# Performance work log

Hardware: AMD Instinct MI355X
Metric: run time of the kernel (lower is better)

Reference implementation:

```python
import jax, jax.numpy as jnp
import numpy as np

U = 100000   # num_users
I = 50000    # num_items
N = U + I    # total nodes
D = 64       # embed_size
L = 3        # n_layers
E = 2000000  # num edges
EPS = 1e-12  # F.normalize default eps


def setup_inputs() -> dict:
    key = jax.random.key(0)
    k1, k2, k3, k4 = jax.random.split(key, 4)
    user_emb = jax.random.normal(k1, (U, D), dtype=jnp.float32) * 0.1
    item_emb = jax.random.normal(k2, (I, D), dtype=jnp.float32) * 0.1
    rows = jax.random.randint(k3, (E,), 0, N, dtype=jnp.int32)
    cols = jax.random.randint(k4, (E,), 0, N, dtype=jnp.int32)
    return {"user_emb": user_emb, "item_emb": item_emb, "rows": rows, "cols": cols}


def _spmm(vals, rows, cols, x):
    # sparse [N,N] @ dense [N,D] via gather + segment reduce
    return jax.ops.segment_sum(vals[:, None] * x[cols], rows, num_segments=N)


def _l2norm(x):
    return x / jnp.maximum(jnp.linalg.norm(x, axis=1, keepdims=True), EPS)


def reference(user_emb, item_emb, rows, cols):
    emb0 = jnp.concatenate([user_emb, item_emb], axis=0)  # [N, D]

    # laplacian_adj: G = D^-1/2 A D^-1/2 on the same edge set
    deg = jax.ops.segment_sum(jnp.ones((E,), emb0.dtype), rows, num_segments=N)
    d_is = jnp.where(deg > 0, deg ** -0.5, 0.0)
    g_vals = d_is[rows] * d_is[cols]  # [E]

    cur = emb0
    acc = emb0
    user_fine, item_fine = [], []
    for _ in range(L):
        gnn = _spmm(g_vals, rows, cols, cur)  # [N, D]
        # fine_laplacian_adj: cosine-sim edge scores, row-normalized
        gr = _l2norm(gnn[rows])
        gc = _l2norm(gnn[cols])
        scores = (jnp.sum(gr * gc, axis=1) + 1.0) * 0.5  # [E] in [0,1]
        rowsum = jax.ops.segment_sum(scores, rows, num_segments=N)
        d_inv = jnp.where(rowsum > 0, 1.0 / rowsum, 0.0)
        fine = _spmm(d_inv[rows] * scores, rows, cols, cur)  # [N, D]
        cur = gnn + fine
        acc = acc + cur
        user_fine.append(fine[:U])
        item_fine.append(fine[U:])

    u_embs = acc[:U]
    i_embs = acc[U:]
    return (u_embs, i_embs, jnp.stack(user_fine, 0), jnp.stack(item_fine, 0))
```

## Files before the change

kernel.cpp:

```cpp
#include <hip/hip_runtime.h>

namespace {

typedef unsigned short u16;
typedef __attribute__((__ext_vector_type__(2))) float f32x2;

constexpr int Un = 100000;
constexpr int In = 50000;
constexpr int Nn = 150000;
constexpr int D  = 64;
constexpr int Ln = 3;
constexpr int En = 2000000;
constexpr int CHUNK = 1024;
constexpr int NB = (Nn + CHUNK - 1) / CHUNK;

__device__ __forceinline__ u16 f2bf(float f) {
    unsigned u = __float_as_uint(f);
    unsigned r = (u + 0x7FFFu + ((u >> 16) & 1u)) >> 16;
    return (u16)r;
}
__device__ __forceinline__ float bflo(unsigned u) {
    return __uint_as_float(u << 16);
}
__device__ __forceinline__ float bfhi(unsigned u) {
    return __uint_as_float(u & 0xFFFF0000u);
}
__device__ __forceinline__ unsigned pack2(float lo, float hi) {
    return (unsigned)f2bf(lo) | ((unsigned)f2bf(hi) << 16);
}

__device__ __forceinline__ f32x2 pkfma(f32x2 a, f32x2 b, f32x2 c) {
    f32x2 d;
    asm("v_pk_fma_f32 %0, %1, %2, %3" : "=v"(d) : "v"(a), "v"(b), "v"(c));
    return d;
}

__device__ __forceinline__ float dpp_add8(float x) {
    x += __uint_as_float((unsigned)__builtin_amdgcn_update_dpp(
        0, (int)__float_as_uint(x), 0xB1, 0xF, 0xF, true));
    x += __uint_as_float((unsigned)__builtin_amdgcn_update_dpp(
        0, (int)__float_as_uint(x), 0x4E, 0xF, 0xF, true));
    x += __uint_as_float((unsigned)__builtin_amdgcn_update_dpp(
        0, (int)__float_as_uint(x), 0x141, 0xF, 0xF, true));
    return x;
}

__device__ __forceinline__ void unp8(uint4 q, f32x2* o) {
    o[0].x = bflo(q.x); o[0].y = bfhi(q.x);
    o[1].x = bflo(q.y); o[1].y = bfhi(q.y);
    o[2].x = bflo(q.z); o[2].y = bfhi(q.z);
    o[3].x = bflo(q.w); o[3].y = bfhi(q.w);
}

__global__ void count_kernel(const int* __restrict__ rows, int* __restrict__ deg,
                             int* __restrict__ eoff) {
    int e = blockIdx.x * blockDim.x + threadIdx.x;
    if (e < En) eoff[e] = atomicAdd(&deg[rows[e]], 1);
}

__global__ void scan_partial(const int* __restrict__ deg, float* __restrict__ d_is,
                             int* __restrict__ bsum) {
    int tid = threadIdx.x;
    int base = blockIdx.x * CHUNK + tid * 4;
    int s = 0;
#pragma unroll
    for (int i = 0; i < 4; ++i) {
        int idx = base + i;
        if (idx < Nn) {
            int d = deg[idx];
            s += d;
            d_is[idx] = d > 0 ? rsqrtf((float)d) : 0.f;
        }
    }
    __shared__ int sh[256];
    sh[tid] = s;
    __syncthreads();
    for (int o = 128; o > 0; o >>= 1) {
        if (tid < o) sh[tid] += sh[tid + o];
        __syncthreads();
    }
    if (tid == 0) bsum[blockIdx.x] = sh[0];
}

__global__ void scan_top(int* __restrict__ bsum, int* __restrict__ row_ptr) {
    __shared__ int sh[256];
    int tid = threadIdx.x;
    int v = (tid < NB) ? bsum[tid] : 0;
    sh[tid] = v;
    __syncthreads();
    for (int o = 1; o < 256; o <<= 1) {
        int t = (tid >= o) ? sh[tid - o] : 0;
        __syncthreads();
        sh[tid] += t;
        __syncthreads();
    }
    if (tid < NB) bsum[tid] = sh[tid] - v;
    if (tid == 255) row_ptr[Nn] = sh[255];
}

__global__ void scan_final(const int* __restrict__ deg, const int* __restrict__ bsum,
                           int* __restrict__ row_ptr) {
    int tid = threadIdx.x;
    int base = blockIdx.x * CHUNK + tid * 4;
    int v[4];
    int ts = 0;
#pragma unroll
    for (int i = 0; i < 4; ++i) {
        int idx = base + i;
        v[i] = (idx < Nn) ? deg[idx] : 0;
        ts += v[i];
    }
    __shared__ int sh[256];
    sh[tid] = ts;
    __syncthreads();
    for (int o = 1; o < 256; o <<= 1) {
        int t = (tid >= o) ? sh[tid - o] : 0;
        __syncthreads();
        sh[tid] += t;
        __syncthreads();
    }
    int excl = bsum[blockIdx.x] + sh[tid] - ts;
#pragma unroll
    for (int i = 0; i < 4; ++i) {
        int idx = base + i;
        if (idx < Nn) row_ptr[idx] = excl;
        excl += v[i];
    }
}

__global__ void fill_kernel(const int* __restrict__ rows, const int* __restrict__ cols,
                            const int* __restrict__ row_ptr, const int* __restrict__ eoff,
                            int* __restrict__ col_off) {
    int e = blockIdx.x * blockDim.x + threadIdx.x;
    if (e >= En) return;
    col_off[row_ptr[rows[e]] + eoff[e]] = cols[e] << 7;
}

__global__ void init_kernel(const float* __restrict__ ue, const float* __restrict__ ie,
                            float* __restrict__ out, u16* __restrict__ cur) {
    int i = (blockIdx.x * 256 + threadIdx.x) * 4;
    if (i >= Nn * D) return;
    const float* src = (i < Un * D) ? (ue + i) : (ie + (i - Un * D));
    float4 v = *(const float4*)src;
    *(float4*)(out + i) = v;
    ushort4 q;
    q.x = f2bf(v.x); q.y = f2bf(v.y); q.z = f2bf(v.z); q.w = f2bf(v.w);
    *(ushort4*)(cur + i) = q;
}

__global__ __launch_bounds__(256) void spmm_gnn(const u16* __restrict__ A_,
                                                u16* __restrict__ Q_,
                                                u16* __restrict__ Qn_,
                                                const int* __restrict__ row_ptr,
                                                const int* __restrict__ col_off,
                                                const float* __restrict__ d_is) {
    int r = (blockIdx.x * 256 + threadIdx.x) >> 6;
    if (r >= Nn) return;
    int lane = threadIdx.x & 63;
    int g = lane >> 3, l = lane & 7;
    unsigned l16 = (unsigned)l * 16u;
    const char* pA = (const char*)A_;
    const char* pd = (const char*)d_is;
    int s = row_ptr[r], t = row_ptr[r + 1];
    float dr = d_is[r];
    f32x2 z; z.x = 0.f; z.y = 0.f;
    f32x2 a2[4] = {z, z, z, z};
    int deg = t - s;
    int nfull = deg >> 3;
    int rem = deg & 7;
    int jb = s + g;
#pragma unroll 2
    for (int i = 0; i < nfull; ++i) {
        unsigned off = (unsigned)col_off[jb + i * 8];
        float dv = *(const float*)(pd + (off >> 5));
        float v = dr * dv;
        uint4 q = *(const uint4*)(pA + (off + l16));
        f32x2 x2[4];
        unp8(q, x2);
        f32x2 v2; v2.x = v; v2.y = v;
#pragma unroll
        for (int p = 0; p < 4; ++p) a2[p] = pkfma(v2, x2[p], a2[p]);
    }
    if (rem) {
        bool valid = g < rem;
        int jc = valid ? (jb + nfull * 8) : s;
        unsigned off = (unsigned)col_off[jc];
        float dv = *(const float*)(pd + (off >> 5));
        float v = valid ? dr * dv : 0.f;
        uint4 q = *(const uint4*)(pA + (off + l16));
        f32x2 x2[4];
        unp8(q, x2);
        f32x2 v2; v2.x = v; v2.y = v;
#pragma unroll
        for (int p = 0; p < 4; ++p) a2[p] = pkfma(v2, x2[p], a2[p]);
    }
    float a[8] = {a2[0].x, a2[0].y, a2[1].x, a2[1].y,
                  a2[2].x, a2[2].y, a2[3].x, a2[3].y};
#pragma unroll
    for (int k = 0; k < 8; ++k) {
        a[k] += __shfl_xor(a[k], 8);
        a[k] += __shfl_xor(a[k], 16);
        a[k] += __shfl_xor(a[k], 32);
    }
    float sq = 0.f;
#pragma unroll
    for (int k = 0; k < 8; ++k) sq = fmaf(a[k], a[k], sq);
    sq = dpp_add8(sq);
    if (g == 0) {
        float ir = 1.f / fmaxf(sqrtf(sq), 1e-12f);
        unsigned ro = ((unsigned)r << 7) + l16;
        uint4 o;
        o.x = pack2(a[0], a[1]); o.y = pack2(a[2], a[3]);
        o.z = pack2(a[4], a[5]); o.w = pack2(a[6], a[7]);
        *(uint4*)((char*)Q_ + ro) = o;
        uint4 on;
        on.x = pack2(a[0] * ir, a[1] * ir); on.y = pack2(a[2] * ir, a[3] * ir);
        on.z = pack2(a[4] * ir, a[5] * ir); on.w = pack2(a[6] * ir, a[7] * ir);
        *(uint4*)((char*)Qn_ + ro) = on;
    }
}

__global__ __launch_bounds__(256) void score_fine_kernel(const u16* __restrict__ A_,
                                                         const u16* __restrict__ Q_,
                                                         const u16* __restrict__ Qn_,
                                                         u16* __restrict__ C_,
                                                         const int* __restrict__ row_ptr,
                                                         const int* __restrict__ col_off,
                                                         float* __restrict__ out, int layer) {
    int r = (blockIdx.x * 256 + threadIdx.x) >> 6;
    if (r >= Nn) return;
    int lane = threadIdx.x & 63;
    int g = lane >> 3, l = lane & 7;
    unsigned l16 = (unsigned)l * 16u;
    const char* pQn = (const char*)Qn_;
    const char* pA  = (const char*)A_;
    int s = row_ptr[r], t = row_ptr[r + 1];
    unsigned ro = ((unsigned)r << 7) + l16;
    uint4 qbn = *(const uint4*)(pQn + ro);
    f32x2 b2[4];
    unp8(qbn, b2);
    f32x2 z; z.x = 0.f; z.y = 0.f;
    f32x2 facc[4] = {z, z, z, z};
    float rowsum = 0.f;
    int deg = t - s;
    int nfull = deg >> 3;
    int rem = deg & 7;
    int jb = s + g;
#pragma unroll 2
    for (int i = 0; i < nfull; ++i) {
        unsigned off = (unsigned)col_off[jb + i * 8];
        unsigned vo = off + l16;
        uint4 qx = *(const uint4*)(pQn + vo);
        uint4 qy = *(const uint4*)(pA + vo);
        f32x2 x2[4];
        unp8(qx, x2);
        f32x2 d2 = pkfma(b2[0], x2[0], z);
        d2 = pkfma(b2[1], x2[1], d2);
        d2 = pkfma(b2[2], x2[2], d2);
        d2 = pkfma(b2[3], x2[3], d2);
        float d = dpp_add8(d2.x + d2.y);
        float sc = fmaf(d, 0.5f, 0.5f);
        rowsum += sc;
        f32x2 y2[4];
        unp8(qy, y2);
        f32x2 sc2; sc2.x = sc; sc2.y = sc;
#pragma unroll
        for (int p = 0; p < 4; ++p) facc[p] = pkfma(sc2, y2[p], facc[p]);
    }
    if (rem) {
        bool valid = g < rem;
        int jc = valid ? (jb + nfull * 8) : s;
        unsigned off = (unsigned)col_off[jc];
        unsigned vo = off + l16;
        uint4 qx = *(const uint4*)(pQn + vo);
        uint4 qy = *(const uint4*)(pA + vo);
        f32x2 x2[4];
        unp8(qx, x2);
        f32x2 d2 = pkfma(b2[0], x2[0], z);
        d2 = pkfma(b2[1], x2[1], d2);
        d2 = pkfma(b2[2], x2[2], d2);
        d2 = pkfma(b2[3], x2[3], d2);
        float d = dpp_add8(d2.x + d2.y);
        float sc = fmaf(d, 0.5f, 0.5f);
        if (!valid) sc = 0.f;
        rowsum += sc;
        f32x2 y2[4];
        unp8(qy, y2);
        f32x2 sc2; sc2.x = sc; sc2.y = sc;
#pragma unroll
        for (int p = 0; p < 4; ++p) facc[p] = pkfma(sc2, y2[p], facc[p]);
    }
    float f[8] = {facc[0].x, facc[0].y, facc[1].x, facc[1].y,
                  facc[2].x, facc[2].y, facc[3].x, facc[3].y};
    rowsum += __shfl_xor(rowsum, 8);
    rowsum += __shfl_xor(rowsum, 16);
    rowsum += __shfl_xor(rowsum, 32);
#pragma unroll
    for (int k = 0; k < 8; ++k) {
        f[k] += __shfl_xor(f[k], 8);
        f[k] += __shfl_xor(f[k], 16);
        f[k] += __shfl_xor(f[k], 32);
    }
    float di = rowsum > 0.f ? 1.f / rowsum : 0.f;
#pragma unroll
    for (int k = 0; k < 8; ++k) f[k] *= di;
    if (g == 0) {
        uint4 qb = *(const uint4*)((const char*)Q_ + ro);
        float b[8] = {bflo(qb.x), bfhi(qb.x), bflo(qb.y), bfhi(qb.y),
                      bflo(qb.z), bfhi(qb.z), bflo(qb.w), bfhi(qb.w)};
        float cn[8];
#pragma unroll
        for (int k = 0; k < 8; ++k) cn[k] = b[k] + f[k];
        uint4 qn;
        qn.x = pack2(cn[0], cn[1]); qn.y = pack2(cn[2], cn[3]);
        qn.z = pack2(cn[4], cn[5]); qn.w = pack2(cn[6], cn[7]);
        *(uint4*)((char*)C_ + ro) = qn;
        float* op = out + (size_t)r * D + l * 8;
        float4 a0 = ((float4*)op)[0], a1 = ((float4*)op)[1];
        a0.x += cn[0]; a0.y += cn[1]; a0.z += cn[2]; a0.w += cn[3];
        a1.x += cn[4]; a1.y += cn[5]; a1.z += cn[6]; a1.w += cn[7];
        ((float4*)op)[0] = a0;
        ((float4*)op)[1] = a1;
        size_t fo;
        if (r < Un)
            fo = (size_t)Nn * D + (size_t)layer * Un * D + (size_t)r * D + l * 8;
        else
            fo = (size_t)Nn * D + (size_t)Ln * Un * D + (size_t)layer * In * D
                 + (size_t)(r - Un) * D + l * 8;
        float4 f0, f1;
        f0.x = f[0]; f0.y = f[1]; f0.z = f[2]; f0.w = f[3];
        f1.x = f[4]; f1.y = f[5]; f1.z = f[6]; f1.w = f[7];
        ((float4*)(out + fo))[0] = f0;
        ((float4*)(out + fo))[1] = f1;
    }
}

}

extern "C" void kernel_launch(void* const* d_in, const int* in_sizes, int n_in,
                              void* d_out, int out_size, void* d_ws, size_t ws_size,
                              hipStream_t stream) {
    const float* user_emb = (const float*)d_in[0];
    const float* item_emb = (const float*)d_in[1];
    const int* rows = (const int*)d_in[2];
    const int* cols = (const int*)d_in[3];
    float* out = (float*)d_out;

    char* ws = (char*)d_ws;
    size_t off = 0;
    auto alloc = [&](size_t bytes) -> void* {
        void* p = ws + off;
        off += (bytes + 255) & ~size_t(255);
        return p;
    };
    u16*   buf0    = (u16*)  alloc((size_t)Nn * D * 2);
    u16*   buf1    = (u16*)  alloc((size_t)Nn * D * 2);
    u16*   buf2    = (u16*)  alloc((size_t)Nn * D * 2);
    u16*   buf3    = (u16*)  alloc((size_t)Nn * D * 2);
    int*   col_off = (int*)  alloc((size_t)(En + 8) * 4);
    int*   deg     = (int*)  alloc((size_t)Nn * 4);
    int*   row_ptr = (int*)  alloc((size_t)(Nn + 1) * 4);
    float* d_is    = (float*)alloc((size_t)Nn * 4);
    int*   bsum    = (int*)  alloc(4096);
    int*   eoff    = (int*)buf2;
    (void)ws_size; (void)in_sizes; (void)n_in; (void)out_size;

    hipMemsetAsync(deg, 0, (size_t)Nn * 4, stream);

    init_kernel<<<(Nn * D / 4 + 255) / 256, 256, 0, stream>>>(user_emb, item_emb, out, buf0);

    const int EB = (En + 255) / 256;
    count_kernel<<<EB, 256, 0, stream>>>(rows, deg, eoff);
    scan_partial<<<NB, 256, 0, stream>>>(deg, d_is, bsum);
    scan_top<<<1, 256, 0, stream>>>(bsum, row_ptr);
    scan_final<<<NB, 256, 0, stream>>>(deg, bsum, row_ptr);
    fill_kernel<<<EB, 256, 0, stream>>>(rows, cols, row_ptr, eoff, col_off);

    const int RB = Nn / 4;
    u16* P = buf0;
    u16* R = buf3;
    for (int l = 0; l < Ln; ++l) {
        spmm_gnn<<<RB, 256, 0, stream>>>(P, buf1, buf2, row_ptr, col_off, d_is);
        score_fine_kernel<<<RB, 256, 0, stream>>>(P, buf1, buf2, R, row_ptr, col_off, out, l);
        u16* tmp = P; P = R; R = tmp;
    }
}
```

Before: 792.9 us.

## Pre-scale features by column degree and reconstruct gnn from normalized vector

Stores a copy of the current embeddings pre-multiplied by D^-1/2 so the gnn SpMM becomes a plain sum, which drops the per-edge d_is gather and multiply. The unnormalized gnn buffer is no longer written; it is rebuilt in the fine kernel as the normalized vector times a stored per-row norm. Tail handling is simplified to predicated loads, and fine outputs use nontemporal stores. In exchange the fine kernel writes an extra scaled buffer per layer, and reconstructing gnn from a bf16-rounded normalized vector may add rounding error.

```diff
diff --git a/kernel.cpp b/kernel.cpp
--- a/kernel.cpp
+++ b/kernel.cpp
@@ -4,6 +4,7 @@
 
 typedef unsigned short u16;
 typedef __attribute__((__ext_vector_type__(2))) float f32x2;
+typedef __attribute__((__ext_vector_type__(4))) float f32x4;
 
 constexpr int Un = 100000;
 constexpr int In = 50000;
@@ -32,6 +33,11 @@
 __device__ __forceinline__ f32x2 pkfma(f32x2 a, f32x2 b, f32x2 c) {
     f32x2 d;
     asm("v_pk_fma_f32 %0, %1, %2, %3" : "=v"(d) : "v"(a), "v"(b), "v"(c));
+    return d;
+}
+__device__ __forceinline__ f32x2 pkadd(f32x2 a, f32x2 b) {
+    f32x2 d;
+    asm("v_pk_add_f32 %0, %1, %2" : "=v"(d) : "v"(a), "v"(b));
     return d;
 }
 
@@ -137,7 +143,9 @@
 }
 
 __global__ void init_kernel(const float* __restrict__ ue, const float* __restrict__ ie,
-                            float* __restrict__ out, u16* __restrict__ cur) {
+                            const float* __restrict__ d_is,
+                            float* __restrict__ out, u16* __restrict__ cur,
+                            u16* __restrict__ S) {
     int i = (blockIdx.x * 256 + threadIdx.x) * 4;
     if (i >= Nn * D) return;
     const float* src = (i < Un * D) ? (ue + i) : (ie + (i - Un * D));
@@ -146,21 +154,25 @@
     ushort4 q;
     q.x = f2bf(v.x); q.y = f2bf(v.y); q.z = f2bf(v.z); q.w = f2bf(v.w);
     *(ushort4*)(cur + i) = q;
-}
-
-__global__ __launch_bounds__(256) void spmm_gnn(const u16* __restrict__ A_,
-                                                u16* __restrict__ Q_,
+    float ds = d_is[i >> 6];
+    ushort4 qs;
+    qs.x = f2bf(v.x * ds); qs.y = f2bf(v.y * ds);
+    qs.z = f2bf(v.z * ds); qs.w = f2bf(v.w * ds);
+    *(ushort4*)(S + i) = qs;
+}
+
+__global__ __launch_bounds__(256) void spmm_gnn(const u16* __restrict__ S_,
                                                 u16* __restrict__ Qn_,
                                                 const int* __restrict__ row_ptr,
                                                 const int* __restrict__ col_off,
-                                                const float* __restrict__ d_is) {
+                                                const float* __restrict__ d_is,
+                                                float* __restrict__ normv) {
     int r = (blockIdx.x * 256 + threadIdx.x) >> 6;
     if (r >= Nn) return;
     int lane = threadIdx.x & 63;
     int g = lane >> 3, l = lane & 7;
     unsigned l16 = (unsigned)l * 16u;
-    const char* pA = (const char*)A_;
-    const char* pd = (const char*)d_is;
+    const char* pS = (const char*)S_;
     int s = row_ptr[r], t = row_ptr[r + 1];
     float dr = d_is[r];
     f32x2 z; z.x = 0.f; z.y = 0.f;
@@ -172,27 +184,19 @@
 #pragma unroll 2
     for (int i = 0; i < nfull; ++i) {
         unsigned off = (unsigned)col_off[jb + i * 8];
-        float dv = *(const float*)(pd + (off >> 5));
-        float v = dr * dv;
-        uint4 q = *(const uint4*)(pA + (off + l16));
+        uint4 q = *(const uint4*)(pS + (off + l16));
         f32x2 x2[4];
         unp8(q, x2);
-        f32x2 v2; v2.x = v; v2.y = v;
-#pragma unroll
-        for (int p = 0; p < 4; ++p) a2[p] = pkfma(v2, x2[p], a2[p]);
-    }
-    if (rem) {
-        bool valid = g < rem;
-        int jc = valid ? (jb + nfull * 8) : s;
-        unsigned off = (unsigned)col_off[jc];
-        float dv = *(const float*)(pd + (off >> 5));
-        float v = valid ? dr * dv : 0.f;
-        uint4 q = *(const uint4*)(pA + (off + l16));
+#pragma unroll
+        for (int p = 0; p < 4; ++p) a2[p] = pkadd(a2[p], x2[p]);
+    }
+    if (g < rem) {
+        unsigned off = (unsigned)col_off[jb + nfull * 8];
+        uint4 q = *(const uint4*)(pS + (off + l16));
         f32x2 x2[4];
         unp8(q, x2);
-        f32x2 v2; v2.x = v; v2.y = v;
-#pragma unroll
-        for (int p = 0; p < 4; ++p) a2[p] = pkfma(v2, x2[p], a2[p]);
+#pragma unroll
+        for (int p = 0; p < 4; ++p) a2[p] = pkadd(a2[p], x2[p]);
     }
     float a[8] = {a2[0].x, a2[0].y, a2[1].x, a2[1].y,
                   a2[2].x, a2[2].y, a2[3].x, a2[3].y};
@@ -207,23 +211,26 @@
     for (int k = 0; k < 8; ++k) sq = fmaf(a[k], a[k], sq);
     sq = dpp_add8(sq);
     if (g == 0) {
-        float ir = 1.f / fmaxf(sqrtf(sq), 1e-12f);
+        float gn = dr * sqrtf(sq);
+        float nrm = fmaxf(gn, 1e-12f);
+        float scale = dr / nrm;
+        normv[r] = nrm;
         unsigned ro = ((unsigned)r << 7) + l16;
-        uint4 o;
-        o.x = pack2(a[0], a[1]); o.y = pack2(a[2], a[3]);
-        o.z = pack2(a[4], a[5]); o.w = pack2(a[6], a[7]);
-        *(uint4*)((char*)Q_ + ro) = o;
         uint4 on;
-        on.x = pack2(a[0] * ir, a[1] * ir); on.y = pack2(a[2] * ir, a[3] * ir);
-        on.z = pack2(a[4] * ir, a[5] * ir); on.w = pack2(a[6] * ir, a[7] * ir);
+        on.x = pack2(a[0] * scale, a[1] * scale);
+        on.y = pack2(a[2] * scale, a[3] * scale);
+        on.z = pack2(a[4] * scale, a[5] * scale);
+        on.w = pack2(a[6] * scale, a[7] * scale);
         *(uint4*)((char*)Qn_ + ro) = on;
     }
 }
 
 __global__ __launch_bounds__(256) void score_fine_kernel(const u16* __restrict__ A_,
-                                                         const u16* __restrict__ Q_,
                                                          const u16* __restrict__ Qn_,
                                                          u16* __restrict__ C_,
+                                                         u16* __restrict__ S_,
+                                                         const float* __restrict__ normv,
+                                                         const float* __restrict__ d_is,
                                                          const int* __restrict__ row_ptr,
                                                          const int* __restrict__ col_off,
                                                          float* __restrict__ out, int layer) {
@@ -237,6 +244,8 @@
     int s = row_ptr[r], t = row_ptr[r + 1];
     unsigned ro = ((unsigned)r << 7) + l16;
     uint4 qbn = *(const uint4*)(pQn + ro);
+    float nrm = normv[r];
+    float dsr = d_is[r];
     f32x2 b2[4];
     unp8(qbn, b2);
     f32x2 z; z.x = 0.f; z.y = 0.f;
@@ -267,10 +276,8 @@
 #pragma unroll
         for (int p = 0; p < 4; ++p) facc[p] = pkfma(sc2, y2[p], facc[p]);
     }
-    if (rem) {
-        bool valid = g < rem;
-        int jc = valid ? (jb + nfull * 8) : s;
-        unsigned off = (unsigned)col_off[jc];
+    if (g < rem) {
+        unsigned off = (unsigned)col_off[jb + nfull * 8];
         unsigned vo = off + l16;
         uint4 qx = *(const uint4*)(pQn + vo);
         uint4 qy = *(const uint4*)(pA + vo);
@@ -282,7 +289,6 @@
         d2 = pkfma(b2[3], x2[3], d2);
         float d = dpp_add8(d2.x + d2.y);
         float sc = fmaf(d, 0.5f, 0.5f);
-        if (!valid) sc = 0.f;
         rowsum += sc;
         f32x2 y2[4];
         unp8(qy, y2);
@@ -305,16 +311,23 @@
 #pragma unroll
     for (int k = 0; k < 8; ++k) f[k] *= di;
     if (g == 0) {
-        uint4 qb = *(const uint4*)((const char*)Q_ + ro);
-        float b[8] = {bflo(qb.x), bfhi(qb.x), bflo(qb.y), bfhi(qb.y),
-                      bflo(qb.z), bfhi(qb.z), bflo(qb.w), bfhi(qb.w)};
+        float bb[8] = {b2[0].x, b2[0].y, b2[1].x, b2[1].y,
+                       b2[2].x, b2[2].y, b2[3].x, b2[3].y};
         float cn[8];
 #pragma unroll
-        for (int k = 0; k < 8; ++k) cn[k] = b[k] + f[k];
+        for (int k = 0; k < 8; ++k) cn[k] = fmaf(bb[k], nrm, f[k]);
         uint4 qn;
         qn.x = pack2(cn[0], cn[1]); qn.y = pack2(cn[2], cn[3]);
         qn.z = pack2(cn[4], cn[5]); qn.w = pack2(cn[6], cn[7]);
         *(uint4*)((char*)C_ + ro) = qn;
+        if (layer != Ln - 1) {
+            uint4 qs;
+            qs.x = pack2(cn[0] * dsr, cn[1] * dsr);
+            qs.y = pack2(cn[2] * dsr, cn[3] * dsr);
+            qs.z = pack2(cn[4] * dsr, cn[5] * dsr);
+            qs.w = pack2(cn[6] * dsr, cn[7] * dsr);
+            *(uint4*)((char*)S_ + ro) = qs;
+        }
         float* op = out + (size_t)r * D + l * 8;
         float4 a0 = ((float4*)op)[0], a1 = ((float4*)op)[1];
         a0.x += cn[0]; a0.y += cn[1]; a0.z += cn[2]; a0.w += cn[3];
@@ -327,11 +340,11 @@
         else
             fo = (size_t)Nn * D + (size_t)Ln * Un * D + (size_t)layer * In * D
                  + (size_t)(r - Un) * D + l * 8;
-        float4 f0, f1;
+        f32x4 f0, f1;
         f0.x = f[0]; f0.y = f[1]; f0.z = f[2]; f0.w = f[3];
         f1.x = f[4]; f1.y = f[5]; f1.z = f[6]; f1.w = f[7];
-        ((float4*)(out + fo))[0] = f0;
-        ((float4*)(out + fo))[1] = f1;
+        __builtin_nontemporal_store(f0, (f32x4*)(out + fo));
+        __builtin_nontemporal_store(f1, (f32x4*)(out + fo) + 1);
     }
 }
 
@@ -361,13 +374,12 @@
     int*   deg     = (int*)  alloc((size_t)Nn * 4);
     int*   row_ptr = (int*)  alloc((size_t)(Nn + 1) * 4);
     float* d_is    = (float*)alloc((size_t)Nn * 4);
+    float* normv   = (float*)alloc((size_t)Nn * 4);
     int*   bsum    = (int*)  alloc(4096);
     int*   eoff    = (int*)buf2;
     (void)ws_size; (void)in_sizes; (void)n_in; (void)out_size;
 
     hipMemsetAsync(deg, 0, (size_t)Nn * 4, stream);
-
-    init_kernel<<<(Nn * D / 4 + 255) / 256, 256, 0, stream>>>(user_emb, item_emb, out, buf0);
 
     const int EB = (En + 255) / 256;
     count_kernel<<<EB, 256, 0, stream>>>(rows, deg, eoff);
@@ -375,13 +387,18 @@
     scan_top<<<1, 256, 0, stream>>>(bsum, row_ptr);
     scan_final<<<NB, 256, 0, stream>>>(deg, bsum, row_ptr);
     fill_kernel<<<EB, 256, 0, stream>>>(rows, cols, row_ptr, eoff, col_off);
+    init_kernel<<<(Nn * D / 4 + 255) / 256, 256, 0, stream>>>(user_emb, item_emb, d_is,
+                                                              out, buf0, buf3);
 
     const int RB = Nn / 4;
     u16* P = buf0;
-    u16* R = buf3;
+    u16* R = buf1;
+    u16* Qn = buf2;
+    u16* S  = buf3;
     for (int l = 0; l < Ln; ++l) {
-        spmm_gnn<<<RB, 256, 0, stream>>>(P, buf1, buf2, row_ptr, col_off, d_is);
-        score_fine_kernel<<<RB, 256, 0, stream>>>(P, buf1, buf2, R, row_ptr, col_off, out, l);
+        spmm_gnn<<<RB, 256, 0, stream>>>(S, Qn, row_ptr, col_off, d_is, normv);
+        score_fine_kernel<<<RB, 256, 0, stream>>>(P, Qn, R, S, normv, d_is,
+                                                  row_ptr, col_off, out, l);
         u16* tmp = P; P = R; R = tmp;
     }
 }
```

After: 788.2 us. No clear change (-0.6%).
